# Optimization experiments

Hardware: AMD Instinct MI355X
Metric: run time of the kernel (lower is better)

Reference implementation:

```python
import jax, jax.numpy as jnp
import numpy as np

DIM = 512
PART = 6
EXP = 4
EPS = 1e-5

def setup_inputs() -> dict:
    key = jax.random.key(0)
    ks = jax.random.split(key, 6)
    B, N = 1024, 162
    x = jax.random.normal(ks[0], (B, N, DIM), dtype=jnp.float32)
    part_tokens = jax.random.normal(ks[1], (PART, DIM), dtype=jnp.float32) * (2.0 / DIM) ** 0.5
    ln_g = jnp.ones((DIM,), dtype=jnp.float32)
    ln_b = jnp.zeros((DIM,), dtype=jnp.float32)
    W1 = jax.random.normal(ks[2], (DIM, EXP * DIM), dtype=jnp.float32) * (1.0 / DIM) ** 0.5
    b1 = jnp.zeros((EXP * DIM,), dtype=jnp.float32)
    W2 = jax.random.normal(ks[3], (EXP * DIM, DIM), dtype=jnp.float32) * (1.0 / (EXP * DIM)) ** 0.5
    b2 = jnp.zeros((DIM,), dtype=jnp.float32)
    return {"x": x, "part_tokens": part_tokens, "ln_g": ln_g, "ln_b": ln_b,
            "W1": W1, "b1": b1, "W2": W2, "b2": b2}

def reference(x, part_tokens, ln_g, ln_b, W1, b1, W2, b2):
    scaling = DIM ** 0.5
    # attention: [P,d] x [B,N,d] -> [B,P,N]
    attn = jnp.einsum('pd,bnd->bpn', part_tokens, x)
    attn = jax.nn.softmax(attn, axis=-1)
    # [B,P,N] x [B,N,d] -> [B,P,d], then post-scale (as in source)
    y = jnp.einsum('bpn,bnd->bpd', attn, x) / scaling
    # FeedForwardBlock: LayerNorm -> Linear -> GELU -> (dropout=identity) -> Linear
    mu = jnp.mean(y, axis=-1, keepdims=True)
    var = jnp.mean(jnp.square(y - mu), axis=-1, keepdims=True)
    h = (y - mu) * jax.lax.rsqrt(var + EPS) * ln_g + ln_b
    h = jax.nn.gelu(h @ W1 + b1, approximate=False)
    return h @ W2 + b2
```

## Files before the change

### kernel.cpp

```cpp
#include <hip/hip_runtime.h>
#include <hip/hip_bf16.h>

constexpr int   DIMC  = 512;
constexpr int   PARTC = 6;
constexpr int   NTOK  = 162;
constexpr float SCALING = 22.62741699796952f;
constexpr float LNEPS   = 1e-5f;

typedef __attribute__((ext_vector_type(8))) short bf16x8;
typedef __attribute__((ext_vector_type(4))) float f32x4;

__global__ __launch_bounds__(256) void transpose_f32_bf16(
    const float* __restrict__ in, __hip_bfloat16* __restrict__ outp, int R, int C)
{
  __shared__ float tile[32][33];
  const int tx = threadIdx.x, ty = threadIdx.y;
  const int bx = blockIdx.x, by = blockIdx.y;
  const int c = bx * 32 + tx;
#pragma unroll
  for (int i = 0; i < 32; i += 8) {
    int r = by * 32 + ty + i;
    tile[ty + i][tx] = in[(size_t)r * C + c];
  }
  __syncthreads();
#pragma unroll
  for (int i = 0; i < 32; i += 8) {
    outp[(size_t)(bx * 32 + ty + i) * R + by * 32 + tx] =
        __float2bfloat16(tile[tx][ty + i]);
  }
}

__global__ __launch_bounds__(256, 3) void attn_ln_k(
    const float* __restrict__ x,
    const float* __restrict__ pt,
    const float* __restrict__ g,
    const float* __restrict__ bta,
    __hip_bfloat16* __restrict__ outp)
{
  const int b = blockIdx.x;
  const int tid = threadIdx.x;
  const int w = tid >> 6;
  const int lane = tid & 63;
  const float* __restrict__ xb = x + (size_t)b * (NTOK * DIMC);

  __shared__ __align__(16) float ulds[2][PARTC][DIMC];
  __shared__ float s_lw[4][PARTC];
  __shared__ float s_red[4][2 * PARTC];

  float4 pA[PARTC], pB[PARTC];
#pragma unroll
  for (int p = 0; p < PARTC; ++p) {
    pA[p] = *(const float4*)(pt + p * DIMC + 8 * lane);
    pB[p] = *(const float4*)(pt + p * DIMC + 8 * lane + 4);
  }

  float u[PARTC][8];
  float l[PARTC];
#pragma unroll
  for (int p = 0; p < PARTC; ++p) {
    l[p] = 0.f;
#pragma unroll
    for (int j = 0; j < 8; ++j) u[p][j] = 0.f;
  }

  for (int n = w; n < NTOK; n += 4) {
    const float* xr = xb + (size_t)n * DIMC + 8 * lane;
    f32x4 xa = __builtin_nontemporal_load((const f32x4*)xr);
    f32x4 xc = __builtin_nontemporal_load((const f32x4*)(xr + 4));

    float acc[PARTC];
#pragma unroll
    for (int p = 0; p < PARTC; ++p) {
      acc[p] = xa[0] * pA[p].x + xa[1] * pA[p].y + xa[2] * pA[p].z + xa[3] * pA[p].w
             + xc[0] * pB[p].x + xc[1] * pB[p].y + xc[2] * pB[p].z + xc[3] * pB[p].w;
    }
#pragma unroll
    for (int off = 32; off > 0; off >>= 1) {
#pragma unroll
      for (int p = 0; p < PARTC; ++p) acc[p] += __shfl_xor(acc[p], off);
    }
#pragma unroll
    for (int p = 0; p < PARTC; ++p) {
      const float we = __expf(acc[p]);
      l[p] += we;
      u[p][0] += we * xa[0]; u[p][1] += we * xa[1];
      u[p][2] += we * xa[2]; u[p][3] += we * xa[3];
      u[p][4] += we * xc[0]; u[p][5] += we * xc[1];
      u[p][6] += we * xc[2]; u[p][7] += we * xc[3];
    }
  }

  if (w >= 2) {
#pragma unroll
    for (int p = 0; p < PARTC; ++p) {
      *(float4*)&ulds[w - 2][p][8 * lane]     = make_float4(u[p][0], u[p][1], u[p][2], u[p][3]);
      *(float4*)&ulds[w - 2][p][8 * lane + 4] = make_float4(u[p][4], u[p][5], u[p][6], u[p][7]);
    }
    if (lane == 0) {
#pragma unroll
      for (int p = 0; p < PARTC; ++p) s_lw[w][p] = l[p];
    }
  }
  __syncthreads();
  if (w < 2) {
#pragma unroll
    for (int p = 0; p < PARTC; ++p) {
      float4 a = *(const float4*)&ulds[w][p][8 * lane];
      float4 c = *(const float4*)&ulds[w][p][8 * lane + 4];
      a.x += u[p][0]; a.y += u[p][1]; a.z += u[p][2]; a.w += u[p][3];
      c.x += u[p][4]; c.y += u[p][5]; c.z += u[p][6]; c.w += u[p][7];
      *(float4*)&ulds[w][p][8 * lane]     = a;
      *(float4*)&ulds[w][p][8 * lane + 4] = c;
    }
    if (lane == 0) {
#pragma unroll
      for (int p = 0; p < PARTC; ++p) s_lw[w][p] = l[p];
    }
  }
  __syncthreads();

  float lt[PARTC];
#pragma unroll
  for (int p = 0; p < PARTC; ++p)
    lt[p] = s_lw[0][p] + s_lw[1][p] + s_lw[2][p] + s_lw[3][p];

  float y0[PARTC], y1[PARTC], s1[PARTC], s2[PARTC];
#pragma unroll
  for (int p = 0; p < PARTC; ++p) {
    const float uu0 = ulds[0][p][2 * tid]     + ulds[1][p][2 * tid];
    const float uu1 = ulds[0][p][2 * tid + 1] + ulds[1][p][2 * tid + 1];
    const float inv = 1.f / (lt[p] * SCALING);
    y0[p] = uu0 * inv;
    y1[p] = uu1 * inv;
    s1[p] = y0[p] + y1[p];
    s2[p] = y0[p] * y0[p] + y1[p] * y1[p];
  }
#pragma unroll
  for (int off = 32; off > 0; off >>= 1) {
#pragma unroll
    for (int p = 0; p < PARTC; ++p) {
      s1[p] += __shfl_xor(s1[p], off);
      s2[p] += __shfl_xor(s2[p], off);
    }
  }
  if (lane == 0) {
#pragma unroll
    for (int p = 0; p < PARTC; ++p) {
      s_red[w][p] = s1[p];
      s_red[w][PARTC + p] = s2[p];
    }
  }
  __syncthreads();

  const float ga0 = g[2 * tid], ga1 = g[2 * tid + 1];
  const float bb0 = bta[2 * tid], bb1 = bta[2 * tid + 1];
  __hip_bfloat16* orow = outp + (size_t)b * PARTC * DIMC;
#pragma unroll
  for (int p = 0; p < PARTC; ++p) {
    float S = s_red[0][p] + s_red[1][p] + s_red[2][p] + s_red[3][p];
    float Q = s_red[0][PARTC + p] + s_red[1][PARTC + p] + s_red[2][PARTC + p] + s_red[3][PARTC + p];
    float mu = S * (1.f / 512.f);
    float var = Q * (1.f / 512.f) - mu * mu;
    float r = rsqrtf(var + LNEPS);
    __hip_bfloat162 hv;
    hv.x = __float2bfloat16((y0[p] - mu) * r * ga0 + bb0);
    hv.y = __float2bfloat16((y1[p] - mu) * r * ga1 + bb1);
    *(__hip_bfloat162*)(orow + p * DIMC + 2 * tid) = hv;
  }
}

template <int BM, int BN, bool GELU>
__global__ __launch_bounds__(256) void gemm_bt(
    const __hip_bfloat16* __restrict__ A,
    const __hip_bfloat16* __restrict__ Bt,
    const float* __restrict__ bias,
    void* __restrict__ Cv,
    int M, int N, int K)
{
  constexpr int BK = 64;
  constexpr int LDT = BK + 16;
  __shared__ __align__(16) unsigned short Al[BM][LDT];
  __shared__ __align__(16) unsigned short Bl[BN][LDT];

  const int tid = threadIdx.x;
  const int w = tid >> 6, lane = tid & 63;
  const int wr = w >> 1, wc = w & 1;
  const int tm = blockIdx.y * BM, tn = blockIdx.x * BN;
  constexpr int FM = BM / 32, FN = BN / 32;

  f32x4 acc[FM][FN];
#pragma unroll
  for (int m = 0; m < FM; ++m)
#pragma unroll
    for (int n = 0; n < FN; ++n) acc[m][n] = (f32x4){0.f, 0.f, 0.f, 0.f};

  const int srow = tid >> 3;
  const int scol = (tid & 7) * 8;

  for (int k0 = 0; k0 < K; k0 += BK) {
    __syncthreads();
#pragma unroll
    for (int r = 0; r < BM / 32; ++r) {
      int row = r * 32 + srow;
      *(int4*)(&Al[row][scol]) =
          *(const int4*)(A + (size_t)(tm + row) * K + k0 + scol);
    }
#pragma unroll
    for (int r = 0; r < BN / 32; ++r) {
      int row = r * 32 + srow;
      *(int4*)(&Bl[row][scol]) =
          *(const int4*)(Bt + (size_t)(tn + row) * K + k0 + scol);
    }
    __syncthreads();

#pragma unroll
    for (int kk = 0; kk < 2; ++kk) {
      const int ko = kk * 32 + (lane >> 4) * 8;
      bf16x8 af[FM], bfr[FN];
#pragma unroll
      for (int m = 0; m < FM; ++m)
        af[m] = *(const bf16x8*)(&Al[wr * (BM / 2) + m * 16 + (lane & 15)][ko]);
#pragma unroll
      for (int n = 0; n < FN; ++n)
        bfr[n] = *(const bf16x8*)(&Bl[wc * (BN / 2) + n * 16 + (lane & 15)][ko]);
#pragma unroll
      for (int m = 0; m < FM; ++m)
#pragma unroll
        for (int n = 0; n < FN; ++n)
          acc[m][n] = __builtin_amdgcn_mfma_f32_16x16x32_bf16(
              af[m], bfr[n], acc[m][n], 0, 0, 0);
    }
  }

  const int cl = lane & 15, rg = (lane >> 4) * 4;
#pragma unroll
  for (int m = 0; m < FM; ++m) {
#pragma unroll
    for (int n = 0; n < FN; ++n) {
      int col = tn + wc * (BN / 2) + n * 16 + cl;
      float bv = bias[col];
#pragma unroll
      for (int r = 0; r < 4; ++r) {
        int row = tm + wr * (BM / 2) + m * 16 + rg + r;
        float v = acc[m][n][r] + bv;
        if (GELU) {
          v = 0.5f * v * (1.f + erff(v * 0.7071067811865476f));
          ((__hip_bfloat16*)Cv)[(size_t)row * N + col] = __float2bfloat16(v);
        } else {
          ((float*)Cv)[(size_t)row * N + col] = v;
        }
      }
    }
  }
}

extern "C" void kernel_launch(void* const* d_in, const int* in_sizes, int n_in,
                              void* d_out, int out_size, void* d_ws, size_t ws_size,
                              hipStream_t stream)
{
  const float* x   = (const float*)d_in[0];
  const float* pt  = (const float*)d_in[1];
  const float* g   = (const float*)d_in[2];
  const float* bta = (const float*)d_in[3];
  const float* W1  = (const float*)d_in[4];
  const float* b1  = (const float*)d_in[5];
  const float* W2  = (const float*)d_in[6];
  const float* b2  = (const float*)d_in[7];
  float* outp = (float*)d_out;

  char* ws = (char*)d_ws;
  __hip_bfloat16* W1T = (__hip_bfloat16*)(ws);
  __hip_bfloat16* W2T = (__hip_bfloat16*)(ws + 2097152);
  __hip_bfloat16* LNO = (__hip_bfloat16*)(ws + 4194304);
  __hip_bfloat16* H   = (__hip_bfloat16*)(ws + 10485760);

  transpose_f32_bf16<<<dim3(2048 / 32, 512 / 32), dim3(32, 8), 0, stream>>>(W1, W1T, 512, 2048);
  transpose_f32_bf16<<<dim3(512 / 32, 2048 / 32), dim3(32, 8), 0, stream>>>(W2, W2T, 2048, 512);

  attn_ln_k<<<1024, 256, 0, stream>>>(x, pt, g, bta, LNO);

  gemm_bt<128, 128, true><<<dim3(2048 / 128, 6144 / 128), 256, 0, stream>>>(
      LNO, W1T, b1, (void*)H, 6144, 2048, 512);

  gemm_bt<128, 64, false><<<dim3(512 / 64, 6144 / 128), 256, 0, stream>>>(
      H, W2T, b2, (void*)outp, 6144, 512, 2048);
}
```

Baseline: 185.9 us.

## Compute attention logits with bf16 MFMA over 16-token tiles instead of shuffle reductions

The per-token dot products between x and the part tokens, which used six cross-lane shuffle reductions per token, are replaced by a 16x16x32 bf16 MFMA over tiles of 16 tokens. Part tokens are staged once in LDS as bf16, and the logits go through LDS before the exp and weighted-accumulation pass. Each x tile is now read twice, once for the MFMA and once for accumulation, and the logits are computed in bf16 precision, which could affect accuracy. The launch-bounds occupancy hint is also raised from 3 to 4 blocks.

```diff
diff --git a/kernel.cpp b/kernel.cpp
--- a/kernel.cpp
+++ b/kernel.cpp
@@ -9,6 +9,13 @@
 
 typedef __attribute__((ext_vector_type(8))) short bf16x8;
 typedef __attribute__((ext_vector_type(4))) float f32x4;
+
+__device__ __forceinline__ unsigned int pack_bf16(float a, float b) {
+  __hip_bfloat16 h0 = __float2bfloat16(a);
+  __hip_bfloat16 h1 = __float2bfloat16(b);
+  return (unsigned int)*(unsigned short*)&h0 |
+         ((unsigned int)*(unsigned short*)&h1 << 16);
+}
 
 __global__ __launch_bounds__(256) void transpose_f32_bf16(
     const float* __restrict__ in, __hip_bfloat16* __restrict__ outp, int R, int C)
@@ -30,7 +37,7 @@
   }
 }
 
-__global__ __launch_bounds__(256, 3) void attn_ln_k(
+__global__ __launch_bounds__(256, 4) void attn_ln_k(
     const float* __restrict__ x,
     const float* __restrict__ pt,
     const float* __restrict__ g,
@@ -41,18 +48,21 @@
   const int tid = threadIdx.x;
   const int w = tid >> 6;
   const int lane = tid & 63;
+  const int tr = lane & 15;
+  const int kh = lane >> 4;
   const float* __restrict__ xb = x + (size_t)b * (NTOK * DIMC);
 
+  __shared__ __align__(16) unsigned short ptl[PARTC][520];
+  __shared__ float s_lg[4][PARTC][16];
   __shared__ __align__(16) float ulds[2][PARTC][DIMC];
   __shared__ float s_lw[4][PARTC];
   __shared__ float s_red[4][2 * PARTC];
 
-  float4 pA[PARTC], pB[PARTC];
-#pragma unroll
-  for (int p = 0; p < PARTC; ++p) {
-    pA[p] = *(const float4*)(pt + p * DIMC + 8 * lane);
-    pB[p] = *(const float4*)(pt + p * DIMC + 8 * lane + 4);
-  }
+  for (int i = tid; i < PARTC * 256; i += 256) {
+    const int p = i >> 8, c2 = (i & 255) * 2;
+    *(unsigned int*)&ptl[p][c2] = pack_bf16(pt[p * DIMC + c2], pt[p * DIMC + c2 + 1]);
+  }
+  __syncthreads();
 
   float u[PARTC][8];
   float l[PARTC];
@@ -63,32 +73,50 @@
     for (int j = 0; j < 8; ++j) u[p][j] = 0.f;
   }
 
-  for (int n = w; n < NTOK; n += 4) {
-    const float* xr = xb + (size_t)n * DIMC + 8 * lane;
-    f32x4 xa = __builtin_nontemporal_load((const f32x4*)xr);
-    f32x4 xc = __builtin_nontemporal_load((const f32x4*)(xr + 4));
-
-    float acc[PARTC];
-#pragma unroll
-    for (int p = 0; p < PARTC; ++p) {
-      acc[p] = xa[0] * pA[p].x + xa[1] * pA[p].y + xa[2] * pA[p].z + xa[3] * pA[p].w
-             + xc[0] * pB[p].x + xc[1] * pB[p].y + xc[2] * pB[p].z + xc[3] * pB[p].w;
-    }
-#pragma unroll
-    for (int off = 32; off > 0; off >>= 1) {
-#pragma unroll
-      for (int p = 0; p < PARTC; ++p) acc[p] += __shfl_xor(acc[p], off);
-    }
-#pragma unroll
-    for (int p = 0; p < PARTC; ++p) {
-      const float we = __expf(acc[p]);
-      l[p] += we;
-      u[p][0] += we * xa[0]; u[p][1] += we * xa[1];
-      u[p][2] += we * xa[2]; u[p][3] += we * xa[3];
-      u[p][4] += we * xc[0]; u[p][5] += we * xc[1];
-      u[p][6] += we * xc[2]; u[p][7] += we * xc[3];
-    }
-  }
+  const int pc = tr < PARTC ? tr : PARTC - 1;
+
+  for (int t = w; t < 11; t += 4) {
+    {
+      const int rowA = min(16 * t + tr, NTOK - 1);
+      const float* __restrict__ xr = xb + (size_t)rowA * DIMC + kh * 8;
+      f32x4 acc4 = (f32x4){0.f, 0.f, 0.f, 0.f};
+#pragma unroll
+      for (int k = 0; k < 16; ++k) {
+        bf16x8 bfr = *(const bf16x8*)&ptl[pc][k * 32 + kh * 8];
+        float4 a = *(const float4*)(xr + k * 32);
+        float4 c = *(const float4*)(xr + k * 32 + 4);
+        union { unsigned int ui[4]; bf16x8 v; } pk;
+        pk.ui[0] = pack_bf16(a.x, a.y);
+        pk.ui[1] = pack_bf16(a.z, a.w);
+        pk.ui[2] = pack_bf16(c.x, c.y);
+        pk.ui[3] = pack_bf16(c.z, c.w);
+        acc4 = __builtin_amdgcn_mfma_f32_16x16x32_bf16(pk.v, bfr, acc4, 0, 0, 0);
+      }
+      if (tr < PARTC) {
+#pragma unroll
+        for (int r = 0; r < 4; ++r) s_lg[w][tr][kh * 4 + r] = acc4[r];
+      }
+    }
+
+    const int tmax = min(16, NTOK - 16 * t);
+    for (int tok = 0; tok < tmax; ++tok) {
+      float we[PARTC];
+#pragma unroll
+      for (int p = 0; p < PARTC; ++p) we[p] = __expf(s_lg[w][p][tok]);
+      const float* xr2 = xb + (size_t)(16 * t + tok) * DIMC + 8 * lane;
+      f32x4 xa = __builtin_nontemporal_load((const f32x4*)xr2);
+      f32x4 xc = __builtin_nontemporal_load((const f32x4*)(xr2 + 4));
+#pragma unroll
+      for (int p = 0; p < PARTC; ++p) {
+        l[p] += we[p];
+        u[p][0] += we[p] * xa[0]; u[p][1] += we[p] * xa[1];
+        u[p][2] += we[p] * xa[2]; u[p][3] += we[p] * xa[3];
+        u[p][4] += we[p] * xc[0]; u[p][5] += we[p] * xc[1];
+        u[p][6] += we[p] * xc[2]; u[p][7] += we[p] * xc[3];
+      }
+    }
+  }
+
 
   if (w >= 2) {
 #pragma unroll
```

New measurement: 207.9 us. 1.12x slower.
